# Kernel optimization log

Measured on AMD Instinct MI355X. Metric: run time of the kernel, lower is better.

Reference implementation:

```python
import jax, jax.numpy as jnp
import numpy as np

B, T, C, H = 2, 2048, 1024, 16
HD = C // H  # head dim = 64


def setup_inputs() -> dict:
    key = jax.random.key(0)
    k1, k2, k3 = jax.random.split(key, 3)
    scale_in = 1.0 / np.sqrt(C)
    x = jax.random.normal(k1, (B, T, C), dtype=jnp.float32)
    w_qkv = jax.random.normal(k2, (C, 3 * C), dtype=jnp.float32) * scale_in
    b_qkv = jnp.zeros((3 * C,), dtype=jnp.float32)
    w_out = jax.random.normal(k3, (C, C), dtype=jnp.float32) * scale_in
    b_out = jnp.zeros((C,), dtype=jnp.float32)
    return {"x": x, "w_qkv": w_qkv, "b_qkv": b_qkv, "w_out": w_out, "b_out": b_out}


def reference(x, w_qkv, b_qkv, w_out, b_out):
    Bq, Tq, Cq = x.shape
    qkv = x @ w_qkv + b_qkv                       # [B,T,3C]
    q, k, v = jnp.split(qkv, 3, axis=-1)          # each [B,T,C]
    # [B,T,C] -> [B,H,T,HD]
    q = q.reshape(Bq, Tq, H, HD).transpose(0, 2, 1, 3)
    k = k.reshape(Bq, Tq, H, HD).transpose(0, 2, 1, 3)
    v = v.reshape(Bq, Tq, H, HD).transpose(0, 2, 1, 3)
    scale = 1.0 / np.sqrt(HD)
    scores = jnp.einsum("bhqd,bhkd->bhqk", q, k) * scale  # [B,H,T,T]
    causal = jnp.tril(jnp.ones((Tq, Tq), dtype=bool))
    scores = jnp.where(causal[None, None], scores, jnp.finfo(scores.dtype).min)
    attn = jax.nn.softmax(scores, axis=-1)
    y = jnp.einsum("bhqk,bhkd->bhqd", attn, v)    # [B,H,T,HD]
    y = y.transpose(0, 2, 1, 3).reshape(Bq, Tq, Cq)
    return y @ w_out + b_out
```

## Files before the change

kernel.cpp:

```cpp
#include <hip/hip_runtime.h>
#include <hip/hip_bf16.h>


#define B_ 2
#define T_ 2048
#define C_ 1024
#define H_ 16
#define HD_ 64
#define M_ (B_ * T_)
#define N3_ (3 * C_)
#define QK2_ 2048
#define QSCALE 0.18033688f

typedef __attribute__((ext_vector_type(8))) short short8;
typedef __attribute__((ext_vector_type(4))) short short4v;
typedef __attribute__((ext_vector_type(4))) float floatx4;

__device__ __forceinline__ unsigned short f2b(float f) {
    __hip_bfloat16 h = __float2bfloat16(f);
    return *reinterpret_cast<unsigned short*>(&h);
}

__device__ __forceinline__ void glds16(const void* g, void* l) {
    __builtin_amdgcn_global_load_lds(
        (const __attribute__((address_space(1))) void*)g,
        (__attribute__((address_space(3))) void*)l, 16, 0, 0);
}

__global__ __launch_bounds__(256) void prep(
    const float* __restrict__ x, const float* __restrict__ w_qkv,
    const float* __restrict__ w_out, unsigned short* __restrict__ xb,
    unsigned short* __restrict__ wt1, unsigned short* __restrict__ wt2) {
    __shared__ float t[64][33];
    const int bi = blockIdx.x;
    const int tid = threadIdx.x;
    if (bi < 4096) {
        int i = (bi * 256 + tid) * 4;
        float4 v = *reinterpret_cast<const float4*>(x + i);
        short4v s;
        s[0] = (short)f2b(v.x); s[1] = (short)f2b(v.y);
        s[2] = (short)f2b(v.z); s[3] = (short)f2b(v.w);
        *reinterpret_cast<short4v*>(xb + i) = s;
        return;
    }
    const float* src; unsigned short* dst; int n0, k0, N;
    if (bi < 4096 + 1536) {
        int u = bi - 4096;
        src = w_qkv; dst = wt1; N = N3_;
        k0 = (u & 15) * 64; n0 = (u >> 4) * 32;
    } else {
        int u = bi - (4096 + 1536);
        src = w_out; dst = wt2; N = C_;
        k0 = (u & 15) * 64; n0 = (u >> 4) * 32;
    }
    const int tx = tid & 31, ty = tid >> 5;
#pragma unroll
    for (int i = 0; i < 8; i++)
        t[ty + i * 8][tx] = src[(size_t)(k0 + ty + i * 8) * N + n0 + tx];
    __syncthreads();
    const int row = tid >> 3;
    const int kp  = (tid & 7) * 8;
    short8 o;
#pragma unroll
    for (int j = 0; j < 8; j++) o[j] = (short)f2b(t[kp + j][row]);
    *reinterpret_cast<short8*>(&dst[(size_t)(n0 + row) * C_ + k0 + kp]) = o;
}

template<int EPI, int BN>
__global__ __launch_bounds__(256) void gemm_glds(
    const unsigned short* __restrict__ A, const unsigned short* __restrict__ Bt,
    const float* __restrict__ bias, void* __restrict__ Cp,
    unsigned short* __restrict__ vtp, int M, int N, int K) {
    constexpr int NI = BN / 32;
    __shared__ __align__(16) unsigned short Al[128 * 64];
    __shared__ __align__(16) unsigned short Bl[BN * 64];

    const int tid  = threadIdx.x;
    const int lane = tid & 63;
    const int w    = tid >> 6;
    const int c16  = lane & 15;
    const int quad = lane >> 4;
    const int NT  = N / BN;
    const int pe  = NT >> 3;
    const int xcd = blockIdx.x & 7;
    const int ii  = blockIdx.x >> 3;
    const int n0  = (xcd * pe + ii % pe) * BN;
    const int m0  = (ii / pe) * 128;
    const int wm = (w >> 1) * 64;
    const int wn = (w & 1) * (BN / 2);

    floatx4 acc[4][NI] = {};

    const int srow = lane >> 3;
    const int sch  = ((lane & 7) ^ srow) * 8;
    const unsigned short* ag = A + (size_t)(m0 + w * 32 + srow) * K + sch;
    const unsigned short* bg = Bt + (size_t)(n0 + w * (BN / 4) + srow) * K + sch;

    const int s7 = c16 & 7;

    for (int k0 = 0; k0 < K; k0 += 64) {
        __syncthreads();
#pragma unroll
        for (int i = 0; i < 4; i++)
            glds16(ag + k0 + (size_t)(i * 8) * K, &Al[(w * 32 + i * 8) * 64]);
#pragma unroll
        for (int i = 0; i < BN / 32; i++)
            glds16(bg + k0 + (size_t)(i * 8) * K,
                   &Bl[(w * (BN / 4) + i * 8) * 64]);
        __syncthreads();

        short8 af[4][2], bf[NI][2];
#pragma unroll
        for (int im = 0; im < 4; im++)
#pragma unroll
            for (int kk = 0; kk < 2; kk++)
                af[im][kk] = *reinterpret_cast<const short8*>(
                    &Al[(wm + im * 16 + c16) * 64 + ((kk * 4 + quad) ^ s7) * 8]);
#pragma unroll
        for (int in = 0; in < NI; in++)
#pragma unroll
            for (int kk = 0; kk < 2; kk++)
                bf[in][kk] = *reinterpret_cast<const short8*>(
                    &Bl[(wn + in * 16 + c16) * 64 + ((kk * 4 + quad) ^ s7) * 8]);
#pragma unroll
        for (int im = 0; im < 4; im++)
#pragma unroll
            for (int in = 0; in < NI; in++)
#pragma unroll
                for (int kk = 0; kk < 2; kk++)
                    acc[im][in] = __builtin_amdgcn_mfma_f32_16x16x32_bf16(
                        af[im][kk], bf[in][kk], acc[im][in], 0, 0, 0);
    }

    const int ncol = n0 + wn;
    float bv[NI];
#pragma unroll
    for (int in = 0; in < NI; in++) bv[in] = bias[ncol + in * 16 + c16];

    if (EPI == 0) {
        float* C = (float*)Cp;
#pragma unroll
        for (int im = 0; im < 4; im++)
#pragma unroll
            for (int r = 0; r < 4; r++) {
                int row = m0 + wm + im * 16 + quad * 4 + r;
#pragma unroll
                for (int in = 0; in < NI; in++)
                    C[(size_t)row * N + ncol + in * 16 + c16] =
                        acc[im][in][r] + bv[in];
            }
    } else {
        if (ncol < 2 * C_) {
            const float fac = (ncol < C_) ? QSCALE : 1.0f;
            unsigned short* qkp = (unsigned short*)Cp;
#pragma unroll
            for (int im = 0; im < 4; im++)
#pragma unroll
                for (int r = 0; r < 4; r++) {
                    int row = m0 + wm + im * 16 + quad * 4 + r;
#pragma unroll
                    for (int in = 0; in < NI; in++)
                        qkp[(size_t)row * QK2_ + ncol + in * 16 + c16] =
                            f2b((acc[im][in][r] + bv[in]) * fac);
                }
        } else {
#pragma unroll
            for (int im = 0; im < 4; im++) {
                int row0 = m0 + wm + im * 16 + quad * 4;
                int b  = row0 >> 11;
                int t0 = row0 & (T_ - 1);
#pragma unroll
                for (int in = 0; in < NI; in++) {
                    int dfull = ncol - 2 * C_ + in * 16 + c16;
                    short4v sv;
#pragma unroll
                    for (int r = 0; r < 4; r++)
                        sv[r] = (short)f2b(acc[im][in][r] + bv[in]);
                    *reinterpret_cast<short4v*>(
                        &vtp[(((size_t)(b << 10) + dfull) << 11) + t0]) = sv;
                }
            }
        }
    }
}

template<bool MASKED>
__device__ __forceinline__ void attn_tile(
    short8 af0, short8 af1,
    const unsigned short* __restrict__ Kb,
    const unsigned short* __restrict__ Vb,
    unsigned short* __restrict__ pw,
    floatx4 O[4], float& l,
    int row0, int kb, int c16, int quad) {
    const floatx4 z = {0.f, 0.f, 0.f, 0.f};
    const int sx  = c16 & 7;
    const int ch0 = (quad ^ sx) * 8;
    const int ch1 = ((quad + 4) ^ sx) * 8;
    floatx4 s[4];
#pragma unroll
    for (int nt = 0; nt < 4; nt++) {
        const int rb = (nt * 16 + c16) * 64;
        short8 k0 = *reinterpret_cast<const short8*>(&Kb[rb + ch0]);
        short8 k1 = *reinterpret_cast<const short8*>(&Kb[rb + ch1]);
        floatx4 t = __builtin_amdgcn_mfma_f32_16x16x32_bf16(k0, af0, z, 0, 0, 0);
        s[nt] = __builtin_amdgcn_mfma_f32_16x16x32_bf16(k1, af1, t, 0, 0, 0);
    }
    const int qrow = row0 + c16;
#pragma unroll
    for (int nt = 0; nt < 4; nt++) {
        short4v p4;
#pragma unroll
        for (int r = 0; r < 4; r++) {
            float p;
            if (MASKED) {
                int key = kb + nt * 16 + quad * 4 + r;
                p = (key <= qrow) ? exp2f(s[nt][r]) : 0.f;
            } else {
                p = exp2f(s[nt][r]);
            }
            l += p;
            p4[r] = (short)f2b(p);
        }
        const int pst = ((2 * nt + (quad >> 1)) ^ sx) * 8 + (quad & 1) * 4;
        *reinterpret_cast<short4v*>(&pw[c16 * 64 + pst]) = p4;
    }
    short8 pf0 = *reinterpret_cast<const short8*>(&pw[c16 * 64 + ch0]);
    short8 pf1 = *reinterpret_cast<const short8*>(&pw[c16 * 64 + ch1]);
#pragma unroll
    for (int nt = 0; nt < 4; nt++) {
        const int rb = (nt * 16 + c16) * 64;
        short8 v0 = *reinterpret_cast<const short8*>(&Vb[rb + ch0]);
        short8 v1 = *reinterpret_cast<const short8*>(&Vb[rb + ch1]);
        floatx4 t = __builtin_amdgcn_mfma_f32_16x16x32_bf16(pf0, v0, O[nt], 0, 0, 0);
        O[nt] = __builtin_amdgcn_mfma_f32_16x16x32_bf16(pf1, v1, t, 0, 0, 0);
    }
}

__global__ __launch_bounds__(512) void attn_mfma(
    const unsigned short* __restrict__ qk,
    const unsigned short* __restrict__ vt,
    unsigned short* __restrict__ y) {
    __shared__ __align__(16) unsigned short Kl[2][64 * 64];
    __shared__ __align__(16) unsigned short Vl[2][64 * 64];
    __shared__ __align__(16) unsigned short Pl[4 * 16 * 64];

    const int tid  = threadIdx.x;
    const int lane = tid & 63;
    const int w    = tid >> 6;
    const int wq   = w & 3;
    const int par  = w >> 2;
    const int c16  = lane & 15;
    const int quad = lane >> 4;
    const int bh = blockIdx.x & 31;
    const int t  = 31 - (blockIdx.x >> 5);
    const int b  = bh >> 4;
    const int h  = bh & 15;
    const int row0 = (4 * t + wq) * 16;
    const int nch  = t + 1;

    const unsigned short* qrow = qk + (size_t)b * T_ * QK2_ + h * HD_;
    const unsigned short* krow = qrow + C_;
    const unsigned short* vrow = vt + ((size_t)bh << 6) * T_;

    short8 af0 = *reinterpret_cast<const short8*>(
        qrow + (size_t)(row0 + c16) * QK2_ + quad * 8);
    short8 af1 = *reinterpret_cast<const short8*>(
        qrow + (size_t)(row0 + c16) * QK2_ + 32 + quad * 8);

    floatx4 O[4] = {};
    float l = 0.f;
    unsigned short* pw = &Pl[wq * 16 * 64];

    const int r8 = lane >> 3;
    const int sw = ((lane & 7) ^ r8) * 8;
    const int srow = w * 8 + r8;

    glds16(krow + (size_t)srow * QK2_ + sw, &Kl[0][(w * 8) * 64]);
    glds16(vrow + (size_t)srow * T_ + sw,   &Vl[0][(w * 8) * 64]);

    for (int c = 0; c < nch; c++) {
        __syncthreads();
        if (c + 1 < nch) {
            const int kb2 = (c + 1) * 64;
            const int nb = (c + 1) & 1;
            glds16(krow + (size_t)(kb2 + srow) * QK2_ + sw, &Kl[nb][(w * 8) * 64]);
            glds16(vrow + (size_t)srow * T_ + kb2 + sw,     &Vl[nb][(w * 8) * 64]);
        }
        if ((c & 1) == par) {
            const int kb = c * 64;
            if (c + 1 < nch)
                attn_tile<false>(af0, af1, Kl[c & 1], Vl[c & 1], pw, O, l,
                                 row0, kb, c16, quad);
            else
                attn_tile<true>(af0, af1, Kl[c & 1], Vl[c & 1], pw, O, l,
                                row0, kb, c16, quad);
        }
    }

    __syncthreads();
    float* Kf = (float*)&Kl[0][0];
    float* Vf = (float*)&Vl[0][0];
    if (par) {
#pragma unroll
        for (int nt = 0; nt < 4; nt++)
            *reinterpret_cast<floatx4*>(&Kf[wq * 1024 + lane * 16 + nt * 4]) = O[nt];
        Vf[wq * 64 + lane] = l;
    }
    __syncthreads();
    if (par == 0) {
#pragma unroll
        for (int nt = 0; nt < 4; nt++)
            O[nt] += *reinterpret_cast<const floatx4*>(
                &Kf[wq * 1024 + lane * 16 + nt * 4]);
        l += Vf[wq * 64 + lane];

        l += __shfl_xor(l, 16);
        l += __shfl_xor(l, 32);
        float lr[4];
#pragma unroll
        for (int r = 0; r < 4; r++)
            lr[r] = __shfl(l, quad * 4 + r);

#pragma unroll
        for (int nt = 0; nt < 4; nt++)
#pragma unroll
            for (int r = 0; r < 4; r++) {
                float val = O[nt][r] / fmaxf(lr[r], 1e-30f);
                y[((size_t)b * T_ + row0 + quad * 4 + r) * C_ + h * HD_ +
                  nt * 16 + c16] = f2b(val);
            }
    }
}

extern "C" void kernel_launch(void* const* d_in, const int* in_sizes, int n_in,
                              void* d_out, int out_size, void* d_ws, size_t ws_size,
                              hipStream_t stream) {
    const float* x     = (const float*)d_in[0];
    const float* w_qkv = (const float*)d_in[1];
    const float* b_qkv = (const float*)d_in[2];
    const float* w_out = (const float*)d_in[3];
    const float* b_out = (const float*)d_in[4];
    float* out = (float*)d_out;

    unsigned short* qkb = (unsigned short*)d_ws;
    unsigned short* vtb = qkb + (size_t)M_ * QK2_;
    unsigned short* yb  = vtb + (size_t)B_ * H_ * HD_ * T_;
    unsigned short* wt1 = yb + (size_t)M_ * C_;
    unsigned short* wt2 = wt1 + (size_t)N3_ * C_;
    unsigned short* xb  = wt2 + (size_t)C_ * C_;

    prep<<<4096 + 1536 + 512, 256, 0, stream>>>(x, w_qkv, w_out, xb, wt1, wt2);

    gemm_glds<1, 128><<<(N3_ / 128) * (M_ / 128), 256, 0, stream>>>(
        xb, wt1, b_qkv, qkb, vtb, M_, N3_, C_);

    attn_mfma<<<B_ * H_ * 32, 512, 0, stream>>>(qkb, vtb, yb);

    gemm_glds<0, 64><<<(C_ / 64) * (M_ / 128), 256, 0, stream>>>(
        yb, wt2, b_out, out, nullptr, M_, C_, C_);
}
```

Baseline: 178.7 us.

## Give each attention wave two 16-row query tiles and halve block size

The attention kernel now runs 256 threads per block, and each wave handles two 16-row query sub-tiles instead of one. Each K/V fragment read from LDS therefore feeds twice as many MFMAs, which cuts LDS traffic per FLOP, and each thread issues two global-to-LDS loads per chunk. It also swaps exp2f for the raw hardware exp2 builtin. The costs are higher register pressure from the doubled accumulators, with launch bounds asking for 4 blocks per CU, and half as many waves per block to hide latency.

```diff
diff --git a/kernel.cpp b/kernel.cpp
--- a/kernel.cpp
+++ b/kernel.cpp
@@ -19,6 +19,14 @@
 __device__ __forceinline__ unsigned short f2b(float f) {
     __hip_bfloat16 h = __float2bfloat16(f);
     return *reinterpret_cast<unsigned short*>(&h);
+}
+
+__device__ __forceinline__ float fexp2(float x) {
+#if __has_builtin(__builtin_amdgcn_exp2f)
+    return __builtin_amdgcn_exp2f(x);
+#else
+    return exp2f(x);
+#endif
 }
 
 __device__ __forceinline__ void glds16(const void* g, void* l) {
@@ -185,58 +193,63 @@
 }
 
 template<bool MASKED>
-__device__ __forceinline__ void attn_tile(
-    short8 af0, short8 af1,
+__device__ __forceinline__ void attn_tile2(
+    const short8 af0[2], const short8 af1[2],
     const unsigned short* __restrict__ Kb,
     const unsigned short* __restrict__ Vb,
     unsigned short* __restrict__ pw,
-    floatx4 O[4], float& l,
+    floatx4 O[2][4], float l[2],
     int row0, int kb, int c16, int quad) {
     const floatx4 z = {0.f, 0.f, 0.f, 0.f};
     const int sx  = c16 & 7;
     const int ch0 = (quad ^ sx) * 8;
     const int ch1 = ((quad + 4) ^ sx) * 8;
-    floatx4 s[4];
 #pragma unroll
     for (int nt = 0; nt < 4; nt++) {
         const int rb = (nt * 16 + c16) * 64;
         short8 k0 = *reinterpret_cast<const short8*>(&Kb[rb + ch0]);
         short8 k1 = *reinterpret_cast<const short8*>(&Kb[rb + ch1]);
-        floatx4 t = __builtin_amdgcn_mfma_f32_16x16x32_bf16(k0, af0, z, 0, 0, 0);
-        s[nt] = __builtin_amdgcn_mfma_f32_16x16x32_bf16(k1, af1, t, 0, 0, 0);
-    }
-    const int qrow = row0 + c16;
-#pragma unroll
-    for (int nt = 0; nt < 4; nt++) {
-        short4v p4;
-#pragma unroll
-        for (int r = 0; r < 4; r++) {
-            float p;
-            if (MASKED) {
-                int key = kb + nt * 16 + quad * 4 + r;
-                p = (key <= qrow) ? exp2f(s[nt][r]) : 0.f;
-            } else {
-                p = exp2f(s[nt][r]);
+#pragma unroll
+        for (int j = 0; j < 2; j++) {
+            floatx4 t = __builtin_amdgcn_mfma_f32_16x16x32_bf16(k0, af0[j], z, 0, 0, 0);
+            floatx4 s = __builtin_amdgcn_mfma_f32_16x16x32_bf16(k1, af1[j], t, 0, 0, 0);
+            short4v p4;
+#pragma unroll
+            for (int r = 0; r < 4; r++) {
+                float p;
+                if (MASKED) {
+                    int key = kb + nt * 16 + quad * 4 + r;
+                    p = (key <= row0 + j * 16 + c16) ? fexp2(s[r]) : 0.f;
+                } else {
+                    p = fexp2(s[r]);
+                }
+                l[j] += p;
+                p4[r] = (short)f2b(p);
             }
-            l += p;
-            p4[r] = (short)f2b(p);
-        }
-        const int pst = ((2 * nt + (quad >> 1)) ^ sx) * 8 + (quad & 1) * 4;
-        *reinterpret_cast<short4v*>(&pw[c16 * 64 + pst]) = p4;
-    }
-    short8 pf0 = *reinterpret_cast<const short8*>(&pw[c16 * 64 + ch0]);
-    short8 pf1 = *reinterpret_cast<const short8*>(&pw[c16 * 64 + ch1]);
+            const int pst = ((2 * nt + (quad >> 1)) ^ sx) * 8 + (quad & 1) * 4;
+            *reinterpret_cast<short4v*>(&pw[j * 1024 + c16 * 64 + pst]) = p4;
+        }
+    }
+    short8 pf0[2], pf1[2];
+#pragma unroll
+    for (int j = 0; j < 2; j++) {
+        pf0[j] = *reinterpret_cast<const short8*>(&pw[j * 1024 + c16 * 64 + ch0]);
+        pf1[j] = *reinterpret_cast<const short8*>(&pw[j * 1024 + c16 * 64 + ch1]);
+    }
 #pragma unroll
     for (int nt = 0; nt < 4; nt++) {
         const int rb = (nt * 16 + c16) * 64;
         short8 v0 = *reinterpret_cast<const short8*>(&Vb[rb + ch0]);
         short8 v1 = *reinterpret_cast<const short8*>(&Vb[rb + ch1]);
-        floatx4 t = __builtin_amdgcn_mfma_f32_16x16x32_bf16(pf0, v0, O[nt], 0, 0, 0);
-        O[nt] = __builtin_amdgcn_mfma_f32_16x16x32_bf16(pf1, v1, t, 0, 0, 0);
-    }
-}
-
-__global__ __launch_bounds__(512) void attn_mfma(
+#pragma unroll
+        for (int j = 0; j < 2; j++) {
+            floatx4 t = __builtin_amdgcn_mfma_f32_16x16x32_bf16(pf0[j], v0, O[j][nt], 0, 0, 0);
+            O[j][nt] = __builtin_amdgcn_mfma_f32_16x16x32_bf16(pf1[j], v1, t, 0, 0, 0);
+        }
+    }
+}
+
+__global__ __launch_bounds__(256, 4) void attn_mfma(
     const unsigned short* __restrict__ qk,
     const unsigned short* __restrict__ vt,
     unsigned short* __restrict__ y) {
@@ -247,53 +260,66 @@
     const int tid  = threadIdx.x;
     const int lane = tid & 63;
     const int w    = tid >> 6;
-    const int wq   = w & 3;
-    const int par  = w >> 2;
+    const int wq   = w & 1;
+    const int par  = w >> 1;
     const int c16  = lane & 15;
     const int quad = lane >> 4;
     const int bh = blockIdx.x & 31;
     const int t  = 31 - (blockIdx.x >> 5);
     const int b  = bh >> 4;
     const int h  = bh & 15;
-    const int row0 = (4 * t + wq) * 16;
+    const int row0 = t * 64 + wq * 32;
     const int nch  = t + 1;
 
     const unsigned short* qrow = qk + (size_t)b * T_ * QK2_ + h * HD_;
     const unsigned short* krow = qrow + C_;
     const unsigned short* vrow = vt + ((size_t)bh << 6) * T_;
 
-    short8 af0 = *reinterpret_cast<const short8*>(
-        qrow + (size_t)(row0 + c16) * QK2_ + quad * 8);
-    short8 af1 = *reinterpret_cast<const short8*>(
-        qrow + (size_t)(row0 + c16) * QK2_ + 32 + quad * 8);
-
-    floatx4 O[4] = {};
-    float l = 0.f;
-    unsigned short* pw = &Pl[wq * 16 * 64];
+    short8 af0[2], af1[2];
+#pragma unroll
+    for (int j = 0; j < 2; j++) {
+        af0[j] = *reinterpret_cast<const short8*>(
+            qrow + (size_t)(row0 + j * 16 + c16) * QK2_ + quad * 8);
+        af1[j] = *reinterpret_cast<const short8*>(
+            qrow + (size_t)(row0 + j * 16 + c16) * QK2_ + 32 + quad * 8);
+    }
+
+    floatx4 O[2][4] = {};
+    float l[2] = {0.f, 0.f};
+    unsigned short* pw = &Pl[wq * 2048];
 
     const int r8 = lane >> 3;
     const int sw = ((lane & 7) ^ r8) * 8;
-    const int srow = w * 8 + r8;
-
-    glds16(krow + (size_t)srow * QK2_ + sw, &Kl[0][(w * 8) * 64]);
-    glds16(vrow + (size_t)srow * T_ + sw,   &Vl[0][(w * 8) * 64]);
+
+#pragma unroll
+    for (int i = 0; i < 2; i++) {
+        glds16(krow + (size_t)(w * 16 + i * 8 + r8) * QK2_ + sw,
+               &Kl[0][(w * 16 + i * 8) * 64]);
+        glds16(vrow + (size_t)(w * 16 + i * 8 + r8) * T_ + sw,
+               &Vl[0][(w * 16 + i * 8) * 64]);
+    }
 
     for (int c = 0; c < nch; c++) {
         __syncthreads();
         if (c + 1 < nch) {
             const int kb2 = (c + 1) * 64;
             const int nb = (c + 1) & 1;
-            glds16(krow + (size_t)(kb2 + srow) * QK2_ + sw, &Kl[nb][(w * 8) * 64]);
-            glds16(vrow + (size_t)srow * T_ + kb2 + sw,     &Vl[nb][(w * 8) * 64]);
+#pragma unroll
+            for (int i = 0; i < 2; i++) {
+                glds16(krow + (size_t)(kb2 + w * 16 + i * 8 + r8) * QK2_ + sw,
+                       &Kl[nb][(w * 16 + i * 8) * 64]);
+                glds16(vrow + (size_t)(w * 16 + i * 8 + r8) * T_ + kb2 + sw,
+                       &Vl[nb][(w * 16 + i * 8) * 64]);
+            }
         }
         if ((c & 1) == par) {
             const int kb = c * 64;
             if (c + 1 < nch)
-                attn_tile<false>(af0, af1, Kl[c & 1], Vl[c & 1], pw, O, l,
+                attn_tile2<false>(af0, af1, Kl[c & 1], Vl[c & 1], pw, O, l,
+                                  row0, kb, c16, quad);
+            else
+                attn_tile2<true>(af0, af1, Kl[c & 1], Vl[c & 1], pw, O, l,
                                  row0, kb, c16, quad);
-            else
-                attn_tile<true>(af0, af1, Kl[c & 1], Vl[c & 1], pw, O, l,
-                                row0, kb, c16, quad);
         }
     }
 
@@ -302,33 +328,40 @@
     float* Vf = (float*)&Vl[0][0];
     if (par) {
 #pragma unroll
-        for (int nt = 0; nt < 4; nt++)
-            *reinterpret_cast<floatx4*>(&Kf[wq * 1024 + lane * 16 + nt * 4]) = O[nt];
-        Vf[wq * 64 + lane] = l;
+        for (int j = 0; j < 2; j++) {
+#pragma unroll
+            for (int nt = 0; nt < 4; nt++)
+                *reinterpret_cast<floatx4*>(
+                    &Kf[(wq * 2 + j) * 1024 + lane * 16 + nt * 4]) = O[j][nt];
+            Vf[(wq * 2 + j) * 64 + lane] = l[j];
+        }
     }
     __syncthreads();
     if (par == 0) {
 #pragma unroll
-        for (int nt = 0; nt < 4; nt++)
-            O[nt] += *reinterpret_cast<const floatx4*>(
-                &Kf[wq * 1024 + lane * 16 + nt * 4]);
-        l += Vf[wq * 64 + lane];
-
-        l += __shfl_xor(l, 16);
-        l += __shfl_xor(l, 32);
-        float lr[4];
-#pragma unroll
-        for (int r = 0; r < 4; r++)
-            lr[r] = __shfl(l, quad * 4 + r);
-
-#pragma unroll
-        for (int nt = 0; nt < 4; nt++)
-#pragma unroll
-            for (int r = 0; r < 4; r++) {
-                float val = O[nt][r] / fmaxf(lr[r], 1e-30f);
-                y[((size_t)b * T_ + row0 + quad * 4 + r) * C_ + h * HD_ +
-                  nt * 16 + c16] = f2b(val);
-            }
+        for (int j = 0; j < 2; j++) {
+#pragma unroll
+            for (int nt = 0; nt < 4; nt++)
+                O[j][nt] += *reinterpret_cast<const floatx4*>(
+                    &Kf[(wq * 2 + j) * 1024 + lane * 16 + nt * 4]);
+            float lj = l[j] + Vf[(wq * 2 + j) * 64 + lane];
+
+            lj += __shfl_xor(lj, 16);
+            lj += __shfl_xor(lj, 32);
+            float lr[4];
+#pragma unroll
+            for (int r = 0; r < 4; r++)
+                lr[r] = __shfl(lj, quad * 4 + r);
+
+#pragma unroll
+            for (int nt = 0; nt < 4; nt++)
+#pragma unroll
+                for (int r = 0; r < 4; r++) {
+                    float val = O[j][nt][r] / fmaxf(lr[r], 1e-30f);
+                    y[((size_t)b * T_ + row0 + j * 16 + quad * 4 + r) * C_ +
+                      h * HD_ + nt * 16 + c16] = f2b(val);
+                }
+        }
     }
 }
 
@@ -354,7 +387,7 @@
     gemm_glds<1, 128><<<(N3_ / 128) * (M_ / 128), 256, 0, stream>>>(
         xb, wt1, b_qkv, qkb, vtb, M_, N3_, C_);
 
-    attn_mfma<<<B_ * H_ * 32, 512, 0, stream>>>(qkb, vtb, yb);
+    attn_mfma<<<B_ * H_ * 32, 256, 0, stream>>>(qkb, vtb, yb);
 
     gemm_glds<0, 64><<<(C_ / 64) * (M_ / 128), 256, 0, stream>>>(
         yb, wt2, b_out, out, nullptr, M_, C_, C_);
```

New measurement: 189.1 us. 1.06x slower.
